# Kernel optimization log

Hardware: AMD Instinct MI355X
Metric: run time of the kernel (lower is better)

Reference implementation:

```python
import jax, jax.numpy as jnp
import numpy as np

EPS = 0.5  # diffusion epsilon from init_kwargs

def setup_inputs() -> dict:
    key = jax.random.key(0)
    k = jax.random.split(key, 7)
    B, N0, N1, n = 1024, 32, 32, 64
    Mu0 = jax.random.normal(k[0], (N0, n), dtype=jnp.float32) * 2.0
    Mu1 = jax.random.normal(k[1], (N1, n), dtype=jnp.float32) * 2.0
    # diagonal covariances must be positive
    S0 = jax.random.uniform(k[2], (N0, n), dtype=jnp.float32, minval=0.1, maxval=1.0)
    S1 = jax.random.uniform(k[3], (N1, n), dtype=jnp.float32, minval=0.1, maxval=1.0)
    Lam = jax.random.uniform(k[4], (N0, N1), dtype=jnp.float32, minval=0.0, maxval=1.0)
    Lam = Lam / Lam.sum()  # transport plan sums to 1
    X = jax.random.normal(k[5], (B, n), dtype=jnp.float32)
    t = jnp.float32(0.3)
    return {"X": X, "Mu0": Mu0, "Mu1": Mu1, "S0": S0, "S1": S1, "Lam": Lam, "t": t}

def reference(X, Mu0, Mu1, S0, S1, Lam, t):
    eps2 = EPS * EPS
    S0e = S0[:, None, :]        # (N0,1,n)
    S1e = S1[None, :, :]        # (1,N1,n)
    Ds = jnp.sqrt(4.0 * S0e * S1e + EPS ** 4)
    Cs = 0.5 * (Ds - eps2)                       # (N0,N1,n)
    mu_t = (1.0 - t) * Mu0[:, None, :] + t * Mu1[None, :, :]  # (N0,N1,n)
    Sigma = (1.0 - t) ** 2 * S0e + t ** 2 * S1e + 2.0 * t * (1.0 - t) * (Cs + 0.5 * eps2)
    # St = Pt - Qt - eps^2 * t
    St = t * S1e + (1.0 - t) * Cs - ((1.0 - t) * S0e + t * Cs) - eps2 * t
    K = St / Sigma                               # (N0,N1,n)
    v = Mu1[None, :, :] - Mu0[:, None, :]        # (N0,N1,n)
    d = X[:, None, None, :] - mu_t               # (B,N0,N1,n)
    U = K * d + v                                # (B,N0,N1,n)
    # diag-Normal log_prob plus n/2*log(2pi) == -0.5*sum(d^2/Sigma + log Sigma)
    logw = -0.5 * jnp.sum(d * d / Sigma + jnp.log(Sigma), axis=-1)  # (B,N0,N1)
    W = jnp.exp(jnp.clip(logw, -50.0, 50.0)) * Lam                  # (B,N0,N1)
    num = jnp.einsum('bijn,bij->bn', U, W)       # (B,n)
    den = jnp.sum(W, axis=(1, 2))[:, None]       # (B,1)
    return num / den
```

## Files before the change

### kernel.cpp

```cpp
#include <hip/hip_runtime.h>
#include <math.h>

#define EPS2f 0.25f
#define EPS4f 0.0625f
#define BB 4

__global__ __launch_bounds__(64) void precomp_kernel(
    const float* __restrict__ Mu0, const float* __restrict__ Mu1,
    const float* __restrict__ S0,  const float* __restrict__ S1,
    const float* __restrict__ tptr,
    float2* __restrict__ AB_T, float2* __restrict__ KV,
    float* __restrict__ C0)
{
    const int ij = blockIdx.x;
    const int k  = threadIdx.x;
    const int i  = ij >> 5;
    const int j  = ij & 31;
    const float t   = *tptr;
    const float omt = 1.0f - t;

    const float s0 = S0[i * 64 + k];
    const float s1 = S1[j * 64 + k];
    const float m0 = Mu0[i * 64 + k];
    const float m1 = Mu1[j * 64 + k];

    const float ds  = sqrtf(4.0f * s0 * s1 + EPS4f);
    const float cs  = 0.5f * (ds - EPS2f);
    const float mt  = omt * m0 + t * m1;
    const float sig = omt * omt * s0 + t * t * s1
                    + 2.0f * t * omt * (cs + 0.5f * EPS2f);
    const float isig = 1.0f / sig;
    const float st = t * s1 - omt * s0 + (omt - t) * cs - EPS2f * t;
    const float kk = st * isig;
    const float v  = m1 - m0;

    AB_T[(k << 10) + ij] = make_float2(isig, 2.0f * mt * isig);
    KV[(ij << 6) + k]    = make_float2(kk, v - kk * mt);

    float c = mt * mt * isig + __logf(sig);
    #pragma unroll
    for (int off = 32; off >= 1; off >>= 1)
        c += __shfl_xor(c, off, 64);
    if (k == 0) C0[ij] = c;
}

__global__ __launch_bounds__(1024, 4) void gmm_main_kernel(
    const float* __restrict__ X,   const float* __restrict__ Lam,
    const float* __restrict__ C0,
    const float2* __restrict__ AB_T, const float2* __restrict__ KV,
    float* __restrict__ out)
{
    __shared__ float4 XsT[64];
    __shared__ float4 Wl[1024];
    __shared__ float  denp[16 * BB];
    __shared__ float  red[16 * 64 * 5];

    const int tid  = threadIdx.x;
    const int lane = tid & 63;
    const int w    = tid >> 6;
    const int b0   = blockIdx.x * BB;

    if (tid < 64 * BB) {
        ((float*)XsT)[(tid & 63) * BB + (tid >> 6)] = X[b0 * 64 + tid];
    }
    __syncthreads();

    const int ij = tid;
    float qa = 0.f, qb = 0.f, qc = 0.f, qd = 0.f;
    #pragma unroll 8
    for (int k = 0; k < 64; ++k) {
        const float2 ab = AB_T[(k << 10) + ij];
        const float4 xk = XsT[k];
        qa = fmaf(fmaf(ab.x, xk.x, -ab.y), xk.x, qa);
        qb = fmaf(fmaf(ab.x, xk.y, -ab.y), xk.y, qb);
        qc = fmaf(fmaf(ab.x, xk.z, -ab.y), xk.z, qc);
        qd = fmaf(fmaf(ab.x, xk.w, -ab.y), xk.w, qd);
    }

    const float c0 = C0[ij], l0 = Lam[ij];
    #define WCALC(q) (__expf(fminf(fmaxf(-0.5f * ((q) + c0), -50.0f), 50.0f)) * l0)
    float4 wv4;
    wv4.x = WCALC(qa); wv4.y = WCALC(qb); wv4.z = WCALC(qc); wv4.w = WCALC(qd);
    #undef WCALC
    Wl[ij] = wv4;

    float d0 = wv4.x, d1 = wv4.y, d2 = wv4.z, d3 = wv4.w;
    #pragma unroll
    for (int off = 32; off >= 1; off >>= 1) {
        d0 += __shfl_xor(d0, off, 64);
        d1 += __shfl_xor(d1, off, 64);
        d2 += __shfl_xor(d2, off, 64);
        d3 += __shfl_xor(d3, off, 64);
    }
    if (lane == 0) {
        denp[w * BB + 0] = d0;
        denp[w * BB + 1] = d1;
        denp[w * BB + 2] = d2;
        denp[w * BB + 3] = d3;
    }

    const float4 xk4 = XsT[lane];
    float n0 = 0.f, n1 = 0.f, n2 = 0.f, n3 = 0.f;
    const int ijbase = w * 64;
    #pragma unroll 8
    for (int c = 0; c < 64; ++c) {
        const int ijb = ijbase + c;
        const float4 wv = Wl[ijb];
        const float2 kv = KV[(ijb << 6) + lane];
        float u;
        u = fmaf(kv.x, xk4.x, kv.y); n0 = fmaf(wv.x, u, n0);
        u = fmaf(kv.x, xk4.y, kv.y); n1 = fmaf(wv.y, u, n1);
        u = fmaf(kv.x, xk4.z, kv.y); n2 = fmaf(wv.z, u, n2);
        u = fmaf(kv.x, xk4.w, kv.y); n3 = fmaf(wv.w, u, n3);
    }
    {
        float* r = &red[(w * 64 + lane) * 5];
        r[0] = n0; r[1] = n1; r[2] = n2; r[3] = n3;
    }
    __syncthreads();

    if (tid < 256) {
        const int bb = tid >> 6;
        const int k  = tid & 63;
        float s = 0.f, d = 0.f;
        #pragma unroll
        for (int ww = 0; ww < 16; ++ww) {
            s += red[(ww * 64 + k) * 5 + bb];
            d += denp[ww * BB + bb];
        }
        out[b0 * 64 + tid] = s / d;
    }
}

extern "C" void kernel_launch(void* const* d_in, const int* in_sizes, int n_in,
                              void* d_out, int out_size, void* d_ws, size_t ws_size,
                              hipStream_t stream) {
    const float* X   = (const float*)d_in[0];
    const float* Mu0 = (const float*)d_in[1];
    const float* Mu1 = (const float*)d_in[2];
    const float* S0  = (const float*)d_in[3];
    const float* S1  = (const float*)d_in[4];
    const float* Lam = (const float*)d_in[5];
    const float* t   = (const float*)d_in[6];
    float* out = (float*)d_out;

    char* ws = (char*)d_ws;
    float2* AB_T = (float2*)(ws);
    float2* KV   = (float2*)(ws + (512 << 10));
    float*  C0   = (float*)(ws + (1024 << 10));

    precomp_kernel<<<1024, 64, 0, stream>>>(Mu0, Mu1, S0, S1, t, AB_T, KV, C0);
    gmm_main_kernel<<<256, 1024, 0, stream>>>(X, Lam, C0, AB_T, KV, out);
}
```

Measured before the change: 84.80 us.

## Fuse per-pair precompute into main kernel, recomputing Gaussian parameters from LDS

Removes the separate precompute kernel and its global workspace arrays, staging S0/Mu0/S1/Mu1 in padded transposed shared memory instead. Each block recomputes sigma, log-sigma, K and the velocity offset on the fly in both the log-weight pass and the numerator pass. This trades a launch and global-memory traffic for redundant transcendental arithmetic in every block and larger LDS use, which may reduce occupancy.

```diff
diff --git a/kernel.cpp b/kernel.cpp
--- a/kernel.cpp
+++ b/kernel.cpp
@@ -3,88 +3,77 @@
 
 #define EPS2f 0.25f
 #define EPS4f 0.0625f
-#define BB 4
 
-__global__ __launch_bounds__(64) void precomp_kernel(
+__global__ __launch_bounds__(1024) void gmm_fused_kernel(
+    const float* __restrict__ X,
     const float* __restrict__ Mu0, const float* __restrict__ Mu1,
     const float* __restrict__ S0,  const float* __restrict__ S1,
-    const float* __restrict__ tptr,
-    float2* __restrict__ AB_T, float2* __restrict__ KV,
-    float* __restrict__ C0)
-{
-    const int ij = blockIdx.x;
-    const int k  = threadIdx.x;
-    const int i  = ij >> 5;
-    const int j  = ij & 31;
-    const float t   = *tptr;
-    const float omt = 1.0f - t;
-
-    const float s0 = S0[i * 64 + k];
-    const float s1 = S1[j * 64 + k];
-    const float m0 = Mu0[i * 64 + k];
-    const float m1 = Mu1[j * 64 + k];
-
-    const float ds  = sqrtf(4.0f * s0 * s1 + EPS4f);
-    const float cs  = 0.5f * (ds - EPS2f);
-    const float mt  = omt * m0 + t * m1;
-    const float sig = omt * omt * s0 + t * t * s1
-                    + 2.0f * t * omt * (cs + 0.5f * EPS2f);
-    const float isig = 1.0f / sig;
-    const float st = t * s1 - omt * s0 + (omt - t) * cs - EPS2f * t;
-    const float kk = st * isig;
-    const float v  = m1 - m0;
-
-    AB_T[(k << 10) + ij] = make_float2(isig, 2.0f * mt * isig);
-    KV[(ij << 6) + k]    = make_float2(kk, v - kk * mt);
-
-    float c = mt * mt * isig + __logf(sig);
-    #pragma unroll
-    for (int off = 32; off >= 1; off >>= 1)
-        c += __shfl_xor(c, off, 64);
-    if (k == 0) C0[ij] = c;
-}
-
-__global__ __launch_bounds__(1024, 4) void gmm_main_kernel(
-    const float* __restrict__ X,   const float* __restrict__ Lam,
-    const float* __restrict__ C0,
-    const float2* __restrict__ AB_T, const float2* __restrict__ KV,
+    const float* __restrict__ Lam, const float* __restrict__ tptr,
     float* __restrict__ out)
 {
-    __shared__ float4 XsT[64];
-    __shared__ float4 Wl[1024];
-    __shared__ float  denp[16 * BB];
+    __shared__ float2 SM0T[64 * 33];
+    __shared__ float2 SM1T[64 * 33];
+    __shared__ float4 Xs4[64];
+    __shared__ float  XsT[4 * 64];
+    __shared__ float  Wl[1024 * 5];
     __shared__ float  red[16 * 64 * 5];
+    __shared__ float  denp[16 * 4];
 
     const int tid  = threadIdx.x;
     const int lane = tid & 63;
     const int w    = tid >> 6;
-    const int b0   = blockIdx.x * BB;
+    const int b0   = blockIdx.x << 2;
 
-    if (tid < 64 * BB) {
-        ((float*)XsT)[(tid & 63) * BB + (tid >> 6)] = X[b0 * 64 + tid];
+    for (int e = tid; e < 2048; e += 1024) {
+        const int i = e >> 6, k = e & 63;
+        SM0T[k * 33 + i] = make_float2(S0[e], Mu0[e]);
+        SM1T[k * 33 + i] = make_float2(S1[e], Mu1[e]);
     }
+    if (tid < 256) {
+        const int bb = tid >> 6, k = tid & 63;
+        const float xv = X[(b0 + bb) * 64 + k];
+        ((float*)&Xs4[k])[bb] = xv;
+        XsT[bb * 64 + k] = xv;
+    }
+
+    const float t    = *tptr;
+    const float omt  = 1.0f - t;
+    const float omt2 = omt * omt, tt = t * t, tt2 = 2.0f * t * omt;
+    const float ctt  = tt2 * 0.125f;
+    const float sc   = omt - t;
+    const float ce   = -EPS2f * t;
+
     __syncthreads();
 
     const int ij = tid;
-    float qa = 0.f, qb = 0.f, qc = 0.f, qd = 0.f;
-    #pragma unroll 8
+    const int ii = ij >> 5, jj = ij & 31;
+    float q0 = 0.f, q1 = 0.f, q2 = 0.f, q3 = 0.f, csum = 0.f;
+    #pragma unroll 4
     for (int k = 0; k < 64; ++k) {
-        const float2 ab = AB_T[(k << 10) + ij];
-        const float4 xk = XsT[k];
-        qa = fmaf(fmaf(ab.x, xk.x, -ab.y), xk.x, qa);
-        qb = fmaf(fmaf(ab.x, xk.y, -ab.y), xk.y, qb);
-        qc = fmaf(fmaf(ab.x, xk.z, -ab.y), xk.z, qc);
-        qd = fmaf(fmaf(ab.x, xk.w, -ab.y), xk.w, qd);
+        const float2 sm0 = SM0T[k * 33 + ii];
+        const float2 sm1 = SM1T[k * 33 + jj];
+        const float4 x   = Xs4[k];
+        const float s0 = sm0.x, m0 = sm0.y, s1 = sm1.x, m1 = sm1.y;
+        const float ds   = sqrtf(fmaf(4.0f * s0, s1, EPS4f));
+        const float cs   = fmaf(0.5f, ds, -0.125f);
+        const float sig  = fmaf(tt2, cs, fmaf(tt, s1, fmaf(omt2, s0, ctt)));
+        const float isig = __builtin_amdgcn_rcpf(sig);
+        const float mt   = fmaf(omt, m0, t * m1);
+        csum += __logf(sig);
+        float dd;
+        dd = x.x - mt; q0 = fmaf(dd * isig, dd, q0);
+        dd = x.y - mt; q1 = fmaf(dd * isig, dd, q1);
+        dd = x.z - mt; q2 = fmaf(dd * isig, dd, q2);
+        dd = x.w - mt; q3 = fmaf(dd * isig, dd, q3);
     }
+    const float lm = Lam[ij];
+    #define WCALC(q) (__expf(fminf(fmaxf(-0.5f * ((q) + csum), -50.f), 50.f)) * lm)
+    const float w0 = WCALC(q0), w1 = WCALC(q1), w2 = WCALC(q2), w3 = WCALC(q3);
+    #undef WCALC
+    Wl[ij * 5 + 0] = w0; Wl[ij * 5 + 1] = w1;
+    Wl[ij * 5 + 2] = w2; Wl[ij * 5 + 3] = w3;
 
-    const float c0 = C0[ij], l0 = Lam[ij];
-    #define WCALC(q) (__expf(fminf(fmaxf(-0.5f * ((q) + c0), -50.0f), 50.0f)) * l0)
-    float4 wv4;
-    wv4.x = WCALC(qa); wv4.y = WCALC(qb); wv4.z = WCALC(qc); wv4.w = WCALC(qd);
-    #undef WCALC
-    Wl[ij] = wv4;
-
-    float d0 = wv4.x, d1 = wv4.y, d2 = wv4.z, d3 = wv4.w;
+    float d0 = w0, d1 = w1, d2 = w2, d3 = w3;
     #pragma unroll
     for (int off = 32; off >= 1; off >>= 1) {
         d0 += __shfl_xor(d0, off, 64);
@@ -93,25 +82,55 @@
         d3 += __shfl_xor(d3, off, 64);
     }
     if (lane == 0) {
-        denp[w * BB + 0] = d0;
-        denp[w * BB + 1] = d1;
-        denp[w * BB + 2] = d2;
-        denp[w * BB + 3] = d3;
+        denp[w * 4 + 0] = d0; denp[w * 4 + 1] = d1;
+        denp[w * 4 + 2] = d2; denp[w * 4 + 3] = d3;
     }
 
-    const float4 xk4 = XsT[lane];
+    const int i0 = w << 1;
+    const float2 a0 = SM0T[lane * 33 + i0];
+    const float2 a1 = SM0T[lane * 33 + i0 + 1];
+    const float xk0 = XsT[0 * 64 + lane], xk1 = XsT[1 * 64 + lane];
+    const float xk2 = XsT[2 * 64 + lane], xk3 = XsT[3 * 64 + lane];
     float n0 = 0.f, n1 = 0.f, n2 = 0.f, n3 = 0.f;
-    const int ijbase = w * 64;
-    #pragma unroll 8
-    for (int c = 0; c < 64; ++c) {
-        const int ijb = ijbase + c;
-        const float4 wv = Wl[ijb];
-        const float2 kv = KV[(ijb << 6) + lane];
-        float u;
-        u = fmaf(kv.x, xk4.x, kv.y); n0 = fmaf(wv.x, u, n0);
-        u = fmaf(kv.x, xk4.y, kv.y); n1 = fmaf(wv.y, u, n1);
-        u = fmaf(kv.x, xk4.z, kv.y); n2 = fmaf(wv.z, u, n2);
-        u = fmaf(kv.x, xk4.w, kv.y); n3 = fmaf(wv.w, u, n3);
+
+    #pragma unroll 4
+    for (int j = 0; j < 32; ++j) {
+        const float2 sm1 = SM1T[lane * 33 + j];
+        const float s1 = sm1.x, m1 = sm1.y;
+        {
+            const float s0 = a0.x, m0 = a0.y;
+            const float ds   = sqrtf(fmaf(4.0f * s0, s1, EPS4f));
+            const float cs   = fmaf(0.5f, ds, -0.125f);
+            const float sig  = fmaf(tt2, cs, fmaf(tt, s1, fmaf(omt2, s0, ctt)));
+            const float isig = __builtin_amdgcn_rcpf(sig);
+            const float st   = fmaf(sc, cs, fmaf(-omt, s0, fmaf(t, s1, ce)));
+            const float kk   = st * isig;
+            const float mt   = fmaf(omt, m0, t * m1);
+            const float vm   = fmaf(-kk, mt, m1 - m0);
+            const int ra = (w * 64 + j) * 5;
+            float u;
+            u = fmaf(kk, xk0, vm); n0 = fmaf(Wl[ra + 0], u, n0);
+            u = fmaf(kk, xk1, vm); n1 = fmaf(Wl[ra + 1], u, n1);
+            u = fmaf(kk, xk2, vm); n2 = fmaf(Wl[ra + 2], u, n2);
+            u = fmaf(kk, xk3, vm); n3 = fmaf(Wl[ra + 3], u, n3);
+        }
+        {
+            const float s0 = a1.x, m0 = a1.y;
+            const float ds   = sqrtf(fmaf(4.0f * s0, s1, EPS4f));
+            const float cs   = fmaf(0.5f, ds, -0.125f);
+            const float sig  = fmaf(tt2, cs, fmaf(tt, s1, fmaf(omt2, s0, ctt)));
+            const float isig = __builtin_amdgcn_rcpf(sig);
+            const float st   = fmaf(sc, cs, fmaf(-omt, s0, fmaf(t, s1, ce)));
+            const float kk   = st * isig;
+            const float mt   = fmaf(omt, m0, t * m1);
+            const float vm   = fmaf(-kk, mt, m1 - m0);
+            const int rb = (w * 64 + 32 + j) * 5;
+            float u;
+            u = fmaf(kk, xk0, vm); n0 = fmaf(Wl[rb + 0], u, n0);
+            u = fmaf(kk, xk1, vm); n1 = fmaf(Wl[rb + 1], u, n1);
+            u = fmaf(kk, xk2, vm); n2 = fmaf(Wl[rb + 2], u, n2);
+            u = fmaf(kk, xk3, vm); n3 = fmaf(Wl[rb + 3], u, n3);
+        }
     }
     {
         float* r = &red[(w * 64 + lane) * 5];
@@ -120,15 +139,14 @@
     __syncthreads();
 
     if (tid < 256) {
-        const int bb = tid >> 6;
-        const int k  = tid & 63;
+        const int bb = tid >> 6, k = tid & 63;
         float s = 0.f, d = 0.f;
         #pragma unroll
         for (int ww = 0; ww < 16; ++ww) {
             s += red[(ww * 64 + k) * 5 + bb];
-            d += denp[ww * BB + bb];
+            d += denp[ww * 4 + bb];
         }
-        out[b0 * 64 + tid] = s / d;
+        out[(b0 + bb) * 64 + k] = s / d;
     }
 }
 
@@ -144,11 +162,5 @@
     const float* t   = (const float*)d_in[6];
     float* out = (float*)d_out;
 
-    char* ws = (char*)d_ws;
-    float2* AB_T = (float2*)(ws);
-    float2* KV   = (float2*)(ws + (512 << 10));
-    float*  C0   = (float*)(ws + (1024 << 10));
-
-    precomp_kernel<<<1024, 64, 0, stream>>>(Mu0, Mu1, S0, S1, t, AB_T, KV, C0);
-    gmm_main_kernel<<<256, 1024, 0, stream>>>(X, Lam, C0, AB_T, KV, out);
+    gmm_fused_kernel<<<256, 1024, 0, stream>>>(X, Mu0, Mu1, S0, S1, Lam, t, out);
 }
```

Result: slower. 102.5 us (+20.8%).
